# Performance work log

Measured on AMD Instinct MI355X. Metric: run time of the kernel, lower is better.

## Reference

```python
import jax, jax.numpy as jnp
import numpy as np

B, S, IN, D, H, L, DFF, C = 64, 256, 32, 512, 8, 2, 2048, 16
DH = D // H


def setup_inputs() -> dict:
    key = jax.random.key(0)
    ks = iter(jax.random.split(key, 40))
    r = lambda shp, s=0.02: (jax.random.normal(next(ks), shp, dtype=jnp.float32) * s)
    inp = {
        'x': jax.random.normal(next(ks), (B, S, IN), dtype=jnp.float32),
        'W_emb': r((IN, D)), 'b_emb': jnp.zeros((D,), jnp.float32),
        'Wq': r((L, D, D)), 'bq': jnp.zeros((L, D), jnp.float32),
        'Wk': r((L, D, D)), 'bk': jnp.zeros((L, D), jnp.float32),
        'Wv': r((L, D, D)), 'bv': jnp.zeros((L, D), jnp.float32),
        'Wo': r((L, D, D)), 'bo': jnp.zeros((L, D), jnp.float32),
        'ln1_s': jnp.ones((L, D), jnp.float32), 'ln1_b': jnp.zeros((L, D), jnp.float32),
        'W1': r((L, D, DFF)), 'b1': jnp.zeros((L, DFF), jnp.float32),
        'W2': r((L, DFF, D)), 'b2': jnp.zeros((L, D), jnp.float32),
        'ln2_s': jnp.ones((L, D), jnp.float32), 'ln2_b': jnp.zeros((L, D), jnp.float32),
        'e1_w': r((D, 128)), 'e1_b': jnp.zeros((128,), jnp.float32),
        'e2_w': r((128, D)), 'e2_b': jnp.zeros((D,), jnp.float32),
        'd1_w': r((D, 128)), 'd1_b': jnp.zeros((128,), jnp.float32),
        'd2_w': r((128, D)), 'd2_b': jnp.zeros((D,), jnp.float32),
        'y': jax.random.randint(next(ks), (B, S, 1), 0, C, dtype=jnp.int32),
    }
    return inp


def _ln(x, s, b):
    m = x.mean(-1, keepdims=True)
    v = ((x - m) ** 2).mean(-1, keepdims=True)
    return (x - m) / jnp.sqrt(v + 1e-5) * s + b


def _ari(a, t, n_cls):
    # adjusted rand index from contingency matrix (labels in [0, n_cls))
    idx = a * n_cls + t
    cm = jnp.zeros((n_cls * n_cls,), jnp.float32).at[idx].add(1.0).reshape(n_cls, n_cls)
    comb2 = lambda m: m * (m - 1.0) * 0.5
    sij = comb2(cm).sum()
    sa = comb2(cm.sum(1)).sum()
    sb = comb2(cm.sum(0)).sum()
    n = jnp.float32(a.shape[0])
    exp = sa * sb / (n * (n - 1.0) * 0.5)
    mx = 0.5 * (sa + sb)
    return (sij - exp) / (mx - exp)


def _net(x, W_emb, b_emb, Wq, bq, Wk, bk, Wv, bv, Wo, bo, ln1_s, ln1_b,
         W1, b1, W2, b2, ln2_s, ln2_b, e1_w, e1_b, e2_w, e2_b, d1_w, d1_b, d2_w, d2_b):
    h = x @ W_emb + b_emb  # [B,S,D]
    for l in range(L):
        q = (h @ Wq[l] + bq[l]).reshape(B, S, H, DH)
        k = (h @ Wk[l] + bk[l]).reshape(B, S, H, DH)
        v = (h @ Wv[l] + bv[l]).reshape(B, S, H, DH)
        scores = jnp.einsum('bqhd,bkhd->bhqk', q, k) / jnp.sqrt(jnp.float32(DH))
        attn = jax.nn.softmax(scores, axis=-1)
        o = jnp.einsum('bhqk,bkhd->bqhd', attn, v).reshape(B, S, D)
        h = _ln(h + o @ Wo[l] + bo[l], ln1_s[l], ln1_b[l])
        f = jax.nn.relu(h @ W1[l] + b1[l]) @ W2[l] + b2[l]
        h = _ln(h + f, ln2_s[l], ln2_b[l])
    enc = jax.nn.relu(h @ e1_w + e1_b) @ e2_w + e2_b
    z = jax.nn.relu(enc @ d1_w + d1_b) @ d2_w + d2_b  # input_to_cluster [B,S,D]
    return z


def reference(x, W_emb, b_emb, Wq, bq, Wk, bk, Wv, bv, Wo, bo, ln1_s, ln1_b,
              W1, b1, W2, b2, ln2_s, ln2_b, e1_w, e1_b, e2_w, e2_b,
              d1_w, d1_b, d2_w, d2_b, y):
    z = _net(x, W_emb, b_emb, Wq, bq, Wk, bk, Wv, bv, Wo, bo, ln1_s, ln1_b,
             W1, b1, W2, b2, ln2_s, ln2_b, e1_w, e1_b, e2_w, e2_b, d1_w, d1_b, d2_w, d2_b)
    # pairwise squared distances across batch per timestep: [S,B,B]
    sq = jnp.sum(z * z, -1)                       # [B,S]
    gram = jnp.einsum('bsd,csd->sbc', z, z)       # [S,B,B]
    dist = sq.T[:, :, None] + sq.T[:, None, :] - 2.0 * gram
    p = jax.nn.softmax(-dist, axis=-1)
    _, knn = jax.lax.top_k(p, C)                  # [S,B,C]
    # tot_sum: rows of dist selected once per i where knn[s,b,i]==i
    counts = jnp.sum(knn == jnp.arange(C)[None, None, :], axis=-1)  # [S,B]
    tot_sum = jnp.sum(dist.sum(-1) * counts.astype(dist.dtype))
    # gather neighbor labels and take mode (ties -> smallest value, like torch.mode)
    y2 = y[..., 0]                                 # [B,S]
    labels = y2[knn, jnp.arange(S)[:, None, None]] # [S,B,C]
    cnt = jnp.sum(labels[..., None] == jnp.arange(C), axis=-2)      # [S,B,C]
    assigned = jnp.argmax(cnt, axis=-1).astype(jnp.int32).reshape(-1)  # S*B (row-major, as torch)
    y_true = y.reshape(-1)                         # B*S (as torch: mismatched order is faithful)
    ari = _ari(assigned, y_true, C)
    return tot_sum, ari, assigned, z
```

## Files before the change

### kernel.cpp

```cpp
#include <hip/hip_runtime.h>
#include <cstdint>
#include <cmath>

#define B_ 64
#define S_ 256
#define IN_ 32
#define D_ 512
#define H_ 8
#define L_ 2
#define DFF_ 2048
#define C_ 16
#define DH_ 64
#define NTOK (B_*S_)
#define HALF_ 8192

typedef __attribute__((ext_vector_type(8))) short bf16x8;
typedef __attribute__((ext_vector_type(4))) float f32x4;
typedef __attribute__((ext_vector_type(8))) ushort ushortx8;

__device__ __forceinline__ ushort bf16_rn(float x) {
    union { float f; uint32_t u; } v; v.f = x;
    uint32_t r = v.u + 0x7fffu + ((v.u >> 16) & 1u);
    return (ushort)(r >> 16);
}
__device__ __forceinline__ float bf16_f32(ushort h) {
    union { uint32_t u; float f; } v; v.u = ((uint32_t)h) << 16;
    return v.f;
}

#define GLDS(gp, lp) __builtin_amdgcn_global_load_lds( \
    (const __attribute__((address_space(1))) void*)(gp), \
    (__attribute__((address_space(3))) void*)(lp), 16, 0, 0)

__device__ __forceinline__ int xcd_swz(int lid, int nwg) {
    return (lid & 7) * (nwg >> 3) + (lid >> 3);
}

template<int MODE>
__global__ __launch_bounds__(256)
void gemm3(const ushort* __restrict__ Ahi, const ushort* __restrict__ Alo,
           const ushort* __restrict__ Bhi, const ushort* __restrict__ Blo,
           const float* __restrict__ bias,
           float* __restrict__ Cf, ushort* __restrict__ Chi, ushort* __restrict__ Clo,
           int M, int N, int K)
{
    __shared__ __align__(16) ushort Als[2][2][128*32];
    __shared__ __align__(16) ushort Bls[2][2][128*32];
    const int tid  = threadIdx.x;
    const int wave = tid >> 6, lane = tid & 63;
    const int nwg = gridDim.x * gridDim.y;
    const int swz = xcd_swz(blockIdx.y * gridDim.x + blockIdx.x, nwg);
    const int m0 = (swz / gridDim.x) << 7, n0 = (swz % gridDim.x) << 7;
    const int wr = wave >> 1, wc = wave & 1;

    const ushort* Ah = Ahi + (size_t)m0 * K;
    const ushort* Al = Alo + (size_t)m0 * K;
    const ushort* Bh = Bhi + (size_t)n0 * K;
    const ushort* Bl = Blo + (size_t)n0 * K;

    const int KT = K >> 5;

    f32x4 acc[4][4];
    #pragma unroll
    for (int m = 0; m < 4; ++m)
        #pragma unroll
        for (int n = 0; n < 4; ++n)
            acc[m][n] = (f32x4){0.f, 0.f, 0.f, 0.f};

    auto stage = [&](int buf, int kk) {
        #pragma unroll
        for (int i = 0; i < 2; ++i) {
            const int rbase = wave * 32 + i * 16;
            const int row   = rbase + (lane >> 2);
            const int slot  = (lane & 3) ^ ((row >> 1) & 3);
            GLDS(Ah + (size_t)row * K + kk + slot * 8, &Als[buf][0][rbase * 32]);
            GLDS(Al + (size_t)row * K + kk + slot * 8, &Als[buf][1][rbase * 32]);
            GLDS(Bh + (size_t)row * K + kk + slot * 8, &Bls[buf][0][rbase * 32]);
            GLDS(Bl + (size_t)row * K + kk + slot * 8, &Bls[buf][1][rbase * 32]);
        }
    };

    stage(0, 0);
    for (int t = 0; t < KT; ++t) {
        const int buf = t & 1;
        if (t + 1 < KT) {
            stage(buf ^ 1, (t + 1) << 5);
            asm volatile("s_waitcnt vmcnt(8)" ::: "memory");
        } else {
            asm volatile("s_waitcnt vmcnt(0)" ::: "memory");
        }
        __builtin_amdgcn_sched_barrier(0);
        __builtin_amdgcn_s_barrier();

        const int chunk = lane >> 4;
        bf16x8 afh[4], afl[4], bfh[4], bfl[4];
        #pragma unroll
        for (int m = 0; m < 4; ++m) {
            const int row = wr * 64 + m * 16 + (lane & 15);
            const int sl  = chunk ^ ((row >> 1) & 3);
            afh[m] = *(const bf16x8*)(&Als[buf][0][row * 32 + sl * 8]);
            afl[m] = *(const bf16x8*)(&Als[buf][1][row * 32 + sl * 8]);
        }
        #pragma unroll
        for (int n = 0; n < 4; ++n) {
            const int row = wc * 64 + n * 16 + (lane & 15);
            const int sl  = chunk ^ ((row >> 1) & 3);
            bfh[n] = *(const bf16x8*)(&Bls[buf][0][row * 32 + sl * 8]);
            bfl[n] = *(const bf16x8*)(&Bls[buf][1][row * 32 + sl * 8]);
        }
        #pragma unroll
        for (int m = 0; m < 4; ++m)
            #pragma unroll
            for (int n = 0; n < 4; ++n) {
                acc[m][n] = __builtin_amdgcn_mfma_f32_16x16x32_bf16(afh[m], bfh[n], acc[m][n], 0, 0, 0);
                acc[m][n] = __builtin_amdgcn_mfma_f32_16x16x32_bf16(afh[m], bfl[n], acc[m][n], 0, 0, 0);
                acc[m][n] = __builtin_amdgcn_mfma_f32_16x16x32_bf16(afl[m], bfh[n], acc[m][n], 0, 0, 0);
            }
        __builtin_amdgcn_sched_barrier(0);
        __builtin_amdgcn_s_barrier();
    }

    const int col_l = lane & 15;
    float bv[4];
    #pragma unroll
    for (int n = 0; n < 4; ++n) bv[n] = bias[n0 + wc * 64 + n * 16 + col_l];
    #pragma unroll
    for (int m = 0; m < 4; ++m) {
        #pragma unroll
        for (int j = 0; j < 4; ++j) {
            const size_t grow = (size_t)(m0 + wr * 64 + m * 16 + (lane >> 4) * 4 + j);
            #pragma unroll
            for (int n = 0; n < 4; ++n) {
                float x = acc[m][n][j] + bv[n];
                if (MODE & 1) x = fmaxf(x, 0.f);
                const size_t gidx = grow * N + (n0 + wc * 64 + n * 16 + col_l);
                if (MODE < 2) {
                    Cf[gidx] = x;
                } else {
                    ushort hb = bf16_rn(x);
                    Chi[gidx] = hb;
                    Clo[gidx] = bf16_rn(x - bf16_f32(hb));
                }
            }
        }
    }
}

__global__ __launch_bounds__(256)
void qk_gemm(const ushort* __restrict__ qkvhi, const ushort* __restrict__ qkvlo,
             float* __restrict__ S)
{
    __shared__ __align__(16) ushort Als[2][2][128*32];
    __shared__ __align__(16) ushort Bls[2][2][128*32];
    const int tid = threadIdx.x, wave = tid >> 6, lane = tid & 63;
    const int swz = xcd_swz(blockIdx.y * 4 + blockIdx.x, 512);
    const int bh = swz >> 2;
    const int qt = (swz >> 1) & 1, kt = swz & 1;
    const int b = bh >> 3, h = bh & 7;
    const ushort* Ah = qkvhi + ((size_t)(b * 256 + qt * 128)) * 1536 + h * 64;
    const ushort* Al = qkvlo + ((size_t)(b * 256 + qt * 128)) * 1536 + h * 64;
    const ushort* Bh = qkvhi + ((size_t)(b * 256 + kt * 128)) * 1536 + 512 + h * 64;
    const ushort* Bl = qkvlo + ((size_t)(b * 256 + kt * 128)) * 1536 + 512 + h * 64;
    const int wr = wave >> 1, wc = wave & 1;

    f32x4 acc[4][4];
    #pragma unroll
    for (int m = 0; m < 4; ++m)
        #pragma unroll
        for (int n = 0; n < 4; ++n)
            acc[m][n] = (f32x4){0.f, 0.f, 0.f, 0.f};

    auto stage = [&](int buf, int kk) {
        #pragma unroll
        for (int i = 0; i < 2; ++i) {
            const int rbase = wave * 32 + i * 16;
            const int row   = rbase + (lane >> 2);
            const int slot  = (lane & 3) ^ ((row >> 1) & 3);
            GLDS(Ah + (size_t)row * 1536 + kk + slot * 8, &Als[buf][0][rbase * 32]);
            GLDS(Al + (size_t)row * 1536 + kk + slot * 8, &Als[buf][1][rbase * 32]);
            GLDS(Bh + (size_t)row * 1536 + kk + slot * 8, &Bls[buf][0][rbase * 32]);
            GLDS(Bl + (size_t)row * 1536 + kk + slot * 8, &Bls[buf][1][rbase * 32]);
        }
    };

    stage(0, 0);
    #pragma unroll
    for (int t = 0; t < 2; ++t) {
        __syncthreads();
        if (t == 0) stage(1, 32);
        const int chunk = lane >> 4;
        bf16x8 afh[4], afl[4], bfh[4], bfl[4];
        #pragma unroll
        for (int m = 0; m < 4; ++m) {
            const int row = wr * 64 + m * 16 + (lane & 15);
            const int sl  = chunk ^ ((row >> 1) & 3);
            afh[m] = *(const bf16x8*)(&Als[t][0][row * 32 + sl * 8]);
            afl[m] = *(const bf16x8*)(&Als[t][1][row * 32 + sl * 8]);
        }
        #pragma unroll
        for (int n = 0; n < 4; ++n) {
            const int row = wc * 64 + n * 16 + (lane & 15);
            const int sl  = chunk ^ ((row >> 1) & 3);
            bfh[n] = *(const bf16x8*)(&Bls[t][0][row * 32 + sl * 8]);
            bfl[n] = *(const bf16x8*)(&Bls[t][1][row * 32 + sl * 8]);
        }
        #pragma unroll
        for (int m = 0; m < 4; ++m)
            #pragma unroll
            for (int n = 0; n < 4; ++n) {
                acc[m][n] = __builtin_amdgcn_mfma_f32_16x16x32_bf16(afh[m], bfh[n], acc[m][n], 0, 0, 0);
                acc[m][n] = __builtin_amdgcn_mfma_f32_16x16x32_bf16(afh[m], bfl[n], acc[m][n], 0, 0, 0);
                acc[m][n] = __builtin_amdgcn_mfma_f32_16x16x32_bf16(afl[m], bfh[n], acc[m][n], 0, 0, 0);
            }
        __syncthreads();
    }

    const int col_l = lane & 15;
    #pragma unroll
    for (int m = 0; m < 4; ++m)
        #pragma unroll
        for (int j = 0; j < 4; ++j) {
            const int row = qt * 128 + wr * 64 + m * 16 + (lane >> 4) * 4 + j;
            #pragma unroll
            for (int n = 0; n < 4; ++n) {
                const int col = kt * 128 + wc * 64 + n * 16 + col_l;
                S[(size_t)bh * 65536 + (size_t)row * 256 + col] = acc[m][n][j] * 0.125f;
            }
        }
}

__global__ __launch_bounds__(256)
void softmax_p(const float* __restrict__ S, ushort* __restrict__ Phi,
               ushort* __restrict__ Plo)
{
    const int row = blockIdx.x * 4 + (threadIdx.x >> 6);
    const int lane = threadIdx.x & 63;
    float4 v = *(const float4*)(S + (size_t)row * 256 + lane * 4);
    float mx = fmaxf(fmaxf(v.x, v.y), fmaxf(v.z, v.w));
    #pragma unroll
    for (int d = 1; d < 64; d <<= 1) mx = fmaxf(mx, __shfl_xor(mx, d));
    float e0 = expf(v.x - mx), e1 = expf(v.y - mx);
    float e2 = expf(v.z - mx), e3 = expf(v.w - mx);
    float s = (e0 + e1) + (e2 + e3);
    #pragma unroll
    for (int d = 1; d < 64; d <<= 1) s += __shfl_xor(s, d);
    const float inv = 1.0f / s;
    float p0 = e0 * inv, p1 = e1 * inv, p2 = e2 * inv, p3 = e3 * inv;
    ushort4 hh, ll;
    hh.x = bf16_rn(p0); ll.x = bf16_rn(p0 - bf16_f32(hh.x));
    hh.y = bf16_rn(p1); ll.y = bf16_rn(p1 - bf16_f32(hh.y));
    hh.z = bf16_rn(p2); ll.z = bf16_rn(p2 - bf16_f32(hh.z));
    hh.w = bf16_rn(p3); ll.w = bf16_rn(p3 - bf16_f32(hh.w));
    *(ushort4*)(Phi + (size_t)row * 256 + lane * 4) = hh;
    *(ushort4*)(Plo + (size_t)row * 256 + lane * 4) = ll;
}

__global__ __launch_bounds__(256)
void vtrans(const ushort* __restrict__ qkvhi, const ushort* __restrict__ qkvlo,
            ushort* __restrict__ VThi, ushort* __restrict__ VTlo)
{
    __shared__ ushort T[64][272];
    const int bh = blockIdx.x;
    const int b = bh >> 3, h = bh & 7;
    const int tid = threadIdx.x;
    #pragma unroll
    for (int pass = 0; pass < 2; ++pass) {
        const ushort* src = pass ? qkvlo : qkvhi;
        ushort* dst = pass ? VTlo : VThi;
        const ushort* p = src + ((size_t)b * 256 + tid) * 1536 + 1024 + h * 64;
        #pragma unroll
        for (int i = 0; i < 8; ++i) {
            ushortx8 v = *(const ushortx8*)(p + i * 8);
            #pragma unroll
            for (int j = 0; j < 8; ++j) T[i * 8 + j][tid] = v[j];
        }
        __syncthreads();
        const int dh = tid >> 2, k0 = (tid & 3) * 64;
        ushort* op = dst + ((size_t)bh * 64 + dh) * 256 + k0;
        #pragma unroll
        for (int i = 0; i < 8; ++i)
            *(ushortx8*)(op + i * 8) = *(const ushortx8*)&T[dh][k0 + i * 8];
        __syncthreads();
    }
}

__global__ __launch_bounds__(256)
void pv_gemm(const ushort* __restrict__ Phi, const ushort* __restrict__ Plo,
             const ushort* __restrict__ VThi, const ushort* __restrict__ VTlo,
             ushort* __restrict__ obhi, ushort* __restrict__ oblo, int t0)
{
    __shared__ __align__(16) ushort Als[2][2][128*32];
    __shared__ __align__(16) ushort Bls[2][2][64*32];
    const int tid = threadIdx.x, wave = tid >> 6, lane = tid & 63;
    const int swz = xcd_swz(blockIdx.y * 2 + blockIdx.x, 256);
    const int bh = swz >> 1, qt = swz & 1;
    const ushort* Ah = Phi + ((size_t)bh * 256 + qt * 128) * 256;
    const ushort* Al = Plo + ((size_t)bh * 256 + qt * 128) * 256;
    const ushort* Bh = VThi + (size_t)bh * 64 * 256;
    const ushort* Bl = VTlo + (size_t)bh * 64 * 256;

    f32x4 acc[2][4];
    #pragma unroll
    for (int m = 0; m < 2; ++m)
        #pragma unroll
        for (int n = 0; n < 4; ++n)
            acc[m][n] = (f32x4){0.f, 0.f, 0.f, 0.f};

    auto stage = [&](int buf, int kk) {
        #pragma unroll
        for (int i = 0; i < 2; ++i) {
            const int rbase = wave * 32 + i * 16;
            const int row   = rbase + (lane >> 2);
            const int slot  = (lane & 3) ^ ((row >> 1) & 3);
            GLDS(Ah + (size_t)row * 256 + kk + slot * 8, &Als[buf][0][rbase * 32]);
            GLDS(Al + (size_t)row * 256 + kk + slot * 8, &Als[buf][1][rbase * 32]);
        }
        const int rbase2 = wave * 16;
        const int row2   = rbase2 + (lane >> 2);
        const int slot2  = (lane & 3) ^ ((row2 >> 1) & 3);
        GLDS(Bh + (size_t)row2 * 256 + kk + slot2 * 8, &Bls[buf][0][rbase2 * 32]);
        GLDS(Bl + (size_t)row2 * 256 + kk + slot2 * 8, &Bls[buf][1][rbase2 * 32]);
    };

    stage(0, 0);
    for (int t = 0; t < 8; ++t) {
        const int buf = t & 1;
        __syncthreads();
        if (t < 7) stage(buf ^ 1, (t + 1) << 5);
        const int chunk = lane >> 4;
        bf16x8 afh[2], afl[2], bfh[4], bfl[4];
        #pragma unroll
        for (int m = 0; m < 2; ++m) {
            const int row = wave * 32 + m * 16 + (lane & 15);
            const int sl  = chunk ^ ((row >> 1) & 3);
            afh[m] = *(const bf16x8*)(&Als[buf][0][row * 32 + sl * 8]);
            afl[m] = *(const bf16x8*)(&Als[buf][1][row * 32 + sl * 8]);
        }
        #pragma unroll
        for (int n = 0; n < 4; ++n) {
            const int row = n * 16 + (lane & 15);
            const int sl  = chunk ^ ((row >> 1) & 3);
            bfh[n] = *(const bf16x8*)(&Bls[buf][0][row * 32 + sl * 8]);
            bfl[n] = *(const bf16x8*)(&Bls[buf][1][row * 32 + sl * 8]);
        }
        #pragma unroll
        for (int m = 0; m < 2; ++m)
            #pragma unroll
            for (int n = 0; n < 4; ++n) {
                acc[m][n] = __builtin_amdgcn_mfma_f32_16x16x32_bf16(afh[m], bfh[n], acc[m][n], 0, 0, 0);
                acc[m][n] = __builtin_amdgcn_mfma_f32_16x16x32_bf16(afh[m], bfl[n], acc[m][n], 0, 0, 0);
                acc[m][n] = __builtin_amdgcn_mfma_f32_16x16x32_bf16(afl[m], bfh[n], acc[m][n], 0, 0, 0);
            }
        __syncthreads();
    }

    const int b = bh >> 3, h = bh & 7;
    const int col_l = lane & 15;
    #pragma unroll
    for (int m = 0; m < 2; ++m)
        #pragma unroll
        for (int j = 0; j < 4; ++j) {
            const int q = qt * 128 + wave * 32 + m * 16 + (lane >> 4) * 4 + j;
            const size_t token = (size_t)t0 + (size_t)b * 256 + q;
            #pragma unroll
            for (int n = 0; n < 4; ++n) {
                const int col = h * 64 + n * 16 + col_l;
                float x = acc[m][n][j];
                ushort hb = bf16_rn(x);
                obhi[token * 512 + col] = hb;
                oblo[token * 512 + col] = bf16_rn(x - bf16_f32(hb));
            }
        }
}

__global__ __launch_bounds__(256)
void gemm_f32(const float* __restrict__ A, const float* __restrict__ W,
              const float* __restrict__ bias, float* __restrict__ Cc,
              ushort* __restrict__ Chi, ushort* __restrict__ Clo,
              int M, int N, int K)
{
    __shared__ float As[16][68];
    __shared__ float Bs[16][64];
    const int tid = threadIdx.x;
    const int tx = tid & 15, ty = tid >> 4;
    const int m0 = blockIdx.y << 6, n0 = blockIdx.x << 6;
    const int arow = tid >> 2, ak4 = (tid & 3) << 2;
    const int brow = tid >> 4, bc4 = (tid & 15) << 2;
    float acc[4][4] = {};
    const float* aptr = A + (size_t)(m0 + arow) * K + ak4;
    const float* bptr = W + (size_t)brow * N + n0 + bc4;
    for (int k0 = 0; k0 < K; k0 += 16) {
        float4 av = *(const float4*)(aptr + k0);
        float4 bv = *(const float4*)(bptr + (size_t)k0 * N);
        __syncthreads();
        As[ak4+0][arow] = av.x; As[ak4+1][arow] = av.y;
        As[ak4+2][arow] = av.z; As[ak4+3][arow] = av.w;
        *(float4*)&Bs[brow][bc4] = bv;
        __syncthreads();
        #pragma unroll
        for (int kk = 0; kk < 16; ++kk) {
            float4 a = *(const float4*)&As[kk][ty << 2];
            float4 b = *(const float4*)&Bs[kk][tx << 2];
            float ar[4] = {a.x,a.y,a.z,a.w};
            float br[4] = {b.x,b.y,b.z,b.w};
            #pragma unroll
            for (int i = 0; i < 4; ++i)
                #pragma unroll
                for (int j = 0; j < 4; ++j)
                    acc[i][j] = fmaf(ar[i], br[j], acc[i][j]);
        }
    }
    float4 bb = *(const float4*)(bias + n0 + (tx << 2));
    #pragma unroll
    for (int i = 0; i < 4; ++i) {
        int m = m0 + (ty << 2) + i;
        float o[4];
        o[0] = acc[i][0] + bb.x; o[1] = acc[i][1] + bb.y;
        o[2] = acc[i][2] + bb.z; o[3] = acc[i][3] + bb.w;
        ushort4 hh, ll;
        hh.x = bf16_rn(o[0]); ll.x = bf16_rn(o[0] - bf16_f32(hh.x));
        hh.y = bf16_rn(o[1]); ll.y = bf16_rn(o[1] - bf16_f32(hh.y));
        hh.z = bf16_rn(o[2]); ll.z = bf16_rn(o[2] - bf16_f32(hh.z));
        hh.w = bf16_rn(o[3]); ll.w = bf16_rn(o[3] - bf16_f32(hh.w));
        const size_t base = (size_t)m * N + n0 + (tx << 2);
        *(float4*)(Cc + base) = (float4){o[0],o[1],o[2],o[3]};
        *(ushort4*)(Chi + base) = hh;
        *(ushort4*)(Clo + base) = ll;
    }
}

__global__ __launch_bounds__(256)
void transpose_split(const float* __restrict__ W, ushort* __restrict__ Thi,
                     ushort* __restrict__ Tlo, int K, int N)
{
    __shared__ float T[64][65];
    const int k0 = blockIdx.y << 6, n0 = blockIdx.x << 6;
    const int tid = threadIdx.x;
    #pragma unroll
    for (int i = 0; i < 16; ++i) {
        int idx = tid + i * 256;
        int kl = idx >> 6, nl = idx & 63;
        T[nl][kl] = W[(size_t)(k0 + kl) * N + n0 + nl];
    }
    __syncthreads();
    #pragma unroll
    for (int i = 0; i < 16; ++i) {
        int idx = tid + i * 256;
        int nl = idx >> 6, kl = idx & 63;
        float x = T[nl][kl];
        ushort hb = bf16_rn(x);
        size_t o = (size_t)(n0 + nl) * K + k0 + kl;
        Thi[o] = hb;
        Tlo[o] = bf16_rn(x - bf16_f32(hb));
    }
}

__global__ __launch_bounds__(256)
void concat3(const float* __restrict__ a, const float* __restrict__ b,
             const float* __restrict__ c, float* __restrict__ out)
{
    int i = blockIdx.x * 256 + threadIdx.x;
    out[i] = (i < 512) ? a[i] : (i < 1024 ? b[i - 512] : c[i - 1024]);
}

__global__ __launch_bounds__(64)
void ln_res(float* __restrict__ h, const float* __restrict__ t,
            const float* __restrict__ sc, const float* __restrict__ bi,
            ushort* __restrict__ hhi, ushort* __restrict__ hlo)
{
    const int row = blockIdx.x, lane = threadIdx.x;
    const size_t off = (size_t)row * D_ + (size_t)lane * 8;
    float x[8];
    float4 a0 = *(const float4*)(h + off),  a1 = *(const float4*)(h + off + 4);
    float4 b0 = *(const float4*)(t + off),  b1 = *(const float4*)(t + off + 4);
    x[0]=a0.x+b0.x; x[1]=a0.y+b0.y; x[2]=a0.z+b0.z; x[3]=a0.w+b0.w;
    x[4]=a1.x+b1.x; x[5]=a1.y+b1.y; x[6]=a1.z+b1.z; x[7]=a1.w+b1.w;

    float s = 0.f;
    #pragma unroll
    for (int i = 0; i < 8; ++i) s += x[i];
    #pragma unroll
    for (int d = 1; d < 64; d <<= 1) s += __shfl_xor(s, d);
    float mean = s * (1.0f / 512.0f);

    float vsum = 0.f;
    #pragma unroll
    for (int i = 0; i < 8; ++i) { float dx = x[i] - mean; vsum += dx * dx; }
    #pragma unroll
    for (int d = 1; d < 64; d <<= 1) vsum += __shfl_xor(vsum, d);
    float den = sqrtf(vsum * (1.0f / 512.0f) + 1e-5f);

    float4 s0 = *(const float4*)(sc + lane*8), s1 = *(const float4*)(sc + lane*8 + 4);
    float4 c0 = *(const float4*)(bi + lane*8), c1 = *(const float4*)(bi + lane*8 + 4);
    float scv[8] = {s0.x,s0.y,s0.z,s0.w,s1.x,s1.y,s1.z,s1.w};
    float biv[8] = {c0.x,c0.y,c0.z,c0.w,c1.x,c1.y,c1.z,c1.w};
    float out[8];
    ushort hh[8], ll[8];
    #pragma unroll
    for (int i = 0; i < 8; ++i) {
        out[i] = (x[i] - mean) / den * scv[i] + biv[i];
        hh[i] = bf16_rn(out[i]);
        ll[i] = bf16_rn(out[i] - bf16_f32(hh[i]));
    }
    *(float4*)(h + off)     = (float4){out[0],out[1],out[2],out[3]};
    *(float4*)(h + off + 4) = (float4){out[4],out[5],out[6],out[7]};
    *(ushort4*)(hhi + off)     = (ushort4){hh[0],hh[1],hh[2],hh[3]};
    *(ushort4*)(hhi + off + 4) = (ushort4){hh[4],hh[5],hh[6],hh[7]};
    *(ushort4*)(hlo + off)     = (ushort4){ll[0],ll[1],ll[2],ll[3]};
    *(ushort4*)(hlo + off + 4) = (ushort4){ll[4],ll[5],ll[6],ll[7]};
}

__global__ __launch_bounds__(64)
void sq_kernel(const float* __restrict__ z, float* __restrict__ sq)
{
#pragma clang fp contract(off)
    const int row = blockIdx.x, lane = threadIdx.x;
    const float* p = z + (size_t)row * D_ + (size_t)lane * 8;
    float4 a0 = *(const float4*)(p), a1 = *(const float4*)(p + 4);
    float s = 0.f;
    float vv[8] = {a0.x,a0.y,a0.z,a0.w,a1.x,a1.y,a1.z,a1.w};
    #pragma unroll
    for (int i = 0; i < 8; ++i) { float t = vv[i] * vv[i]; s = s + t; }
    #pragma unroll
    for (int d = 1; d < 64; d <<= 1) s += __shfl_xor(s, d);
    if (lane == 0) sq[row] = s;
}

__global__ __launch_bounds__(256)
void copy_z(const float* __restrict__ z, float* __restrict__ out)
{
    size_t i4 = (size_t)blockIdx.x * 256 + threadIdx.x;
    if (i4 < (size_t)NTOK * D_ / 4) {
        float4 t = ((const float4*)z)[i4];
        out[i4*4+0] = t.x; out[i4*4+1] = t.y;
        out[i4*4+2] = t.z; out[i4*4+3] = t.w;
    }
}

__global__ __launch_bounds__(256)
void gram_kernel(const float* __restrict__ z, float* __restrict__ gram)
{
    __shared__ float Ls[16][68];
    const int s = blockIdx.x;
    const int tid = threadIdx.x;
    const int tx = tid & 15, ty = tid >> 4;
    const int arow = tid >> 2, ak4 = (tid & 3) << 2;
    float acc[4][4] = {};
    const float* zp = z + ((size_t)arow * S_ + s) * D_ + ak4;
    for (int k0 = 0; k0 < D_; k0 += 16) {
        float4 av = *(const float4*)(zp + k0);
        __syncthreads();
        Ls[ak4+0][arow] = av.x; Ls[ak4+1][arow] = av.y;
        Ls[ak4+2][arow] = av.z; Ls[ak4+3][arow] = av.w;
        __syncthreads();
        #pragma unroll
        for (int kk = 0; kk < 16; ++kk) {
            float4 a = *(const float4*)&Ls[kk][ty << 2];
            float4 b = *(const float4*)&Ls[kk][tx << 2];
            float ar[4] = {a.x,a.y,a.z,a.w};
            float br[4] = {b.x,b.y,b.z,b.w};
            #pragma unroll
            for (int i = 0; i < 4; ++i)
                #pragma unroll
                for (int j = 0; j < 4; ++j)
                    acc[i][j] = fmaf(ar[i], br[j], acc[i][j]);
        }
    }
    #pragma unroll
    for (int i = 0; i < 4; ++i) {
        float4 o = {acc[i][0], acc[i][1], acc[i][2], acc[i][3]};
        *(float4*)(gram + ((size_t)s * 64 + (ty<<2) + i) * 64 + (tx<<2)) = o;
    }
}

__global__ __launch_bounds__(64)
void cluster_kernel(const float* __restrict__ gram, const float* __restrict__ sq,
                    const int* __restrict__ y, float* __restrict__ contrib,
                    int* __restrict__ assigned, float* __restrict__ out_assigned_f)
{
#pragma clang fp contract(off)
    __shared__ float G[64][65];
    __shared__ float sqs[64];
    const int s = blockIdx.x, b = threadIdx.x;
    for (int i = b; i < 4096; i += 64)
        G[i >> 6][i & 63] = gram[(size_t)s * 4096 + i];
    sqs[b] = sq[(size_t)b * S_ + s];
    __syncthreads();

    const float sqb = sqs[b];
    float dmin = INFINITY, dsum = 0.f;
    for (int c = 0; c < 64; ++c) {
        float d = sqb + sqs[c] - 2.0f * G[b][c];
        dmin = fminf(dmin, d);
        dsum = dsum + d;
    }
    float Z = 0.f;
    for (int c = 0; c < 64; ++c) {
        float d = sqb + sqs[c] - 2.0f * G[b][c];
        float e = expf(dmin - d);
        G[b][c] = e;
        Z = Z + e;
    }
    for (int c = 0; c < 64; ++c) G[b][c] = G[b][c] / Z;

    int knn[16];
    #pragma unroll
    for (int j = 0; j < 16; ++j) {
        float bp = -1.f; int bi2 = 0;
        for (int c = 0; c < 64; ++c) {
            float pv = G[b][c];
            if (pv > bp) { bp = pv; bi2 = c; }
        }
        knn[j] = bi2;
        G[b][bi2] = -1.f;
    }
    int cmatch = 0;
    #pragma unroll
    for (int j = 0; j < 16; ++j) cmatch += (knn[j] == j) ? 1 : 0;
    int lab[16];
    #pragma unroll
    for (int j = 0; j < 16; ++j) lab[j] = y[knn[j] * S_ + s];
    int bestc = -1, bestcls = 0;
    #pragma unroll
    for (int cls = 0; cls < 16; ++cls) {
        int cc = 0;
        #pragma unroll
        for (int j = 0; j < 16; ++j) cc += (lab[j] == cls) ? 1 : 0;
        if (cc > bestc) { bestc = cc; bestcls = cls; }
    }
    const int oi = s * 64 + b;
    contrib[oi] = dsum * (float)cmatch;
    assigned[oi] = bestcls;
    out_assigned_f[oi] = (float)bestcls;
}

__global__ __launch_bounds__(256)
void finalize_kernel(const float* __restrict__ contrib, const int* __restrict__ assigned,
                     const int* __restrict__ y, float* __restrict__ dout)
{
#pragma clang fp contract(off)
    __shared__ int cm[256];
    __shared__ float red[256];
    const int tid = threadIdx.x;
    cm[tid] = 0;
    float s = 0.f;
    for (int i = tid; i < NTOK; i += 256) s = s + contrib[i];
    red[tid] = s;
    __syncthreads();
    for (int i = tid; i < NTOK; i += 256)
        atomicAdd(&cm[assigned[i] * 16 + y[i]], 1);
    __syncthreads();
    for (int st = 128; st > 0; st >>= 1) {
        if (tid < st) red[tid] = red[tid] + red[tid + st];
        __syncthreads();
    }
    if (tid == 0) {
        dout[0] = red[0];
        float sij = 0.f, sa = 0.f, sb = 0.f;
        for (int i = 0; i < 256; ++i) {
            float mm = (float)cm[i];
            sij = sij + mm * (mm - 1.0f) * 0.5f;
        }
        for (int r = 0; r < 16; ++r) {
            int rs = 0;
            for (int c2 = 0; c2 < 16; ++c2) rs += cm[r * 16 + c2];
            float mm = (float)rs;
            sa = sa + mm * (mm - 1.0f) * 0.5f;
        }
        for (int c2 = 0; c2 < 16; ++c2) {
            int cs = 0;
            for (int r = 0; r < 16; ++r) cs += cm[r * 16 + c2];
            float mm = (float)cs;
            sb = sb + mm * (mm - 1.0f) * 0.5f;
        }
        float n = 16384.0f;
        float expv = sa * sb / (n * (n - 1.0f) * 0.5f);
        float mx = 0.5f * (sa + sb);
        dout[1] = (sij - expv) / (mx - expv);
    }
}

extern "C" void kernel_launch(void* const* d_in, const int* in_sizes, int n_in,
                              void* d_out, int out_size, void* d_ws, size_t ws_size,
                              hipStream_t stream)
{
    (void)in_sizes; (void)n_in; (void)out_size; (void)ws_size;
    const float* x     = (const float*)d_in[0];
    const float* W_emb = (const float*)d_in[1];
    const float* b_emb = (const float*)d_in[2];
    const float* Wq    = (const float*)d_in[3];
    const float* bq    = (const float*)d_in[4];
    const float* Wk    = (const float*)d_in[5];
    const float* bk    = (const float*)d_in[6];
    const float* Wv    = (const float*)d_in[7];
    const float* bv    = (const float*)d_in[8];
    const float* Wo    = (const float*)d_in[9];
    const float* bo    = (const float*)d_in[10];
    const float* ln1_s = (const float*)d_in[11];
    const float* ln1_b = (const float*)d_in[12];
    const float* W1    = (const float*)d_in[13];
    const float* b1    = (const float*)d_in[14];
    const float* W2    = (const float*)d_in[15];
    const float* b2    = (const float*)d_in[16];
    const float* ln2_s = (const float*)d_in[17];
    const float* ln2_b = (const float*)d_in[18];
    const float* e1_w  = (const float*)d_in[19];
    const float* e1_b  = (const float*)d_in[20];
    const float* e2_w  = (const float*)d_in[21];
    const float* e2_b  = (const float*)d_in[22];
    const float* d1_w  = (const float*)d_in[23];
    const float* d1_b  = (const float*)d_in[24];
    const float* d2_w  = (const float*)d_in[25];
    const float* d2_b  = (const float*)d_in[26];
    const int*   y     = (const int*)d_in[27];

    float* ws = (float*)d_ws;
    float*  h    = ws;
    ushort* hhi  = (ushort*)(ws + 8388608);
    ushort* hlo  = (ushort*)(ws + 12582912);
    float*  SCR  = ws + 16777216;
    ushort* obhi = (ushort*)(ws + 37748736);
    ushort* oblo = (ushort*)(ws + 41943040);
    float*  wt   = ws + 46137344;
    ushort* WTQKV_HI = (ushort*)wt;
    ushort* WTQKV_LO = WTQKV_HI + 786432;
    ushort* WTO_HI   = WTQKV_LO + 786432;
    ushort* WTO_LO   = WTO_HI + 262144;
    ushort* WT1_HI   = WTO_LO + 262144;
    ushort* WT1_LO   = WT1_HI + 1048576;
    ushort* WT2_HI   = WT1_LO + 1048576;
    ushort* WT2_LO   = WT2_HI + 1048576;
    ushort* WE1_HI   = WT2_LO + 1048576;
    ushort* WE1_LO   = WE1_HI + 65536;
    ushort* WE2_HI   = WE1_LO + 65536;
    ushort* WE2_LO   = WE2_HI + 65536;
    ushort* WD1_HI   = WE2_LO + 65536;
    ushort* WD1_LO   = WD1_HI + 65536;
    ushort* WD2_HI   = WD1_LO + 65536;
    ushort* WD2_LO   = WD2_HI + 65536;
    float*  biasqkv  = ws + 49545216;

    float*  Sb    = SCR;
    ushort* qkvhi = (ushort*)(SCR + 8388608);
    ushort* qkvlo = (ushort*)(SCR + 11534336);
    ushort* VThi  = (ushort*)(SCR + 14680064);
    ushort* VTlo  = (ushort*)(SCR + 15728640);
    ushort* Phi_  = (ushort*)(SCR + 8388608);
    ushort* Plo_  = (ushort*)(SCR + 16777216);
    float*  Of32  = SCR;
    ushort* f1hi  = (ushort*)SCR;
    ushort* f1lo  = (ushort*)(SCR + 8388608);
    float*  Xhalf = SCR + 16777216;
    ushort* enchi = (ushort*)SCR;
    ushort* enclo = (ushort*)(SCR + 4194304);
    float*  z     = SCR + 8388608;
    float*  gram  = SCR + 16777216;
    float*  sqb_  = SCR + 17825792;
    float*  contrib = SCR + 17842176;
    int*    assigned = (int*)(SCR + 17858560);
    ushort* t1hi = obhi;
    ushort* t1lo = oblo;
    ushort* t2hi = obhi + 2097152;
    ushort* t2lo = oblo + 2097152;
    float*  dout = (float*)d_out;

    dim3 blk(256);
    auto gg = [](int M, int N) { return dim3(N >> 7, M >> 7); };

    transpose_split<<<dim3(2, 8), blk, 0, stream>>>(e1_w, WE1_HI, WE1_LO, 512, 128);
    transpose_split<<<dim3(8, 2), blk, 0, stream>>>(e2_w, WE2_HI, WE2_LO, 128, 512);
    transpose_split<<<dim3(2, 8), blk, 0, stream>>>(d1_w, WD1_HI, WD1_LO, 512, 128);
    transpose_split<<<dim3(8, 2), blk, 0, stream>>>(d2_w, WD2_HI, WD2_LO, 128, 512);

    gemm_f32<<<dim3(8, 256), blk, 0, stream>>>(x, W_emb, b_emb, h, hhi, hlo, NTOK, D_, IN_);

    for (int l = 0; l < L_; ++l) {
        transpose_split<<<dim3(8, 8), blk, 0, stream>>>(Wq + (size_t)l*D_*D_, WTQKV_HI,            WTQKV_LO,            512, 512);
        transpose_split<<<dim3(8, 8), blk, 0, stream>>>(Wk + (size_t)l*D_*D_, WTQKV_HI + 512*512,  WTQKV_LO + 512*512,  512, 512);
        transpose_split<<<dim3(8, 8), blk, 0, stream>>>(Wv + (size_t)l*D_*D_, WTQKV_HI + 1024*512, WTQKV_LO + 1024*512, 512, 512);
        transpose_split<<<dim3(8, 8), blk, 0, stream>>>(Wo + (size_t)l*D_*D_, WTO_HI, WTO_LO, 512, 512);
        transpose_split<<<dim3(32, 8), blk, 0, stream>>>(W1 + (size_t)l*D_*DFF_, WT1_HI, WT1_LO, 512, 2048);
        transpose_split<<<dim3(8, 32), blk, 0, stream>>>(W2 + (size_t)l*DFF_*D_, WT2_HI, WT2_LO, 2048, 512);
        concat3<<<dim3(6), blk, 0, stream>>>(bq + l*D_, bk + l*D_, bv + l*D_, biasqkv);

        for (int qtr = 0; qtr < 4; ++qtr) {
            const size_t hoff = (size_t)qtr * 4096 * 512;
            gemm3<2><<<gg(4096, 1536), blk, 0, stream>>>(
                hhi + hoff, hlo + hoff, WTQKV_HI, WTQKV_LO, biasqkv,
                nullptr, qkvhi, qkvlo, 4096, 1536, 512);
            vtrans<<<dim3(128), blk, 0, stream>>>(qkvhi, qkvlo, VThi, VTlo);
            qk_gemm<<<dim3(4, 128), blk, 0, stream>>>(qkvhi, qkvlo, Sb);
            softmax_p<<<dim3(8192), blk, 0, stream>>>(Sb, Phi_, Plo_);
            pv_gemm<<<dim3(2, 128), blk, 0, stream>>>(Phi_, Plo_, VThi, VTlo,
                                                      obhi, oblo, qtr * 4096);
        }
        gemm3<0><<<gg(NTOK, 512), blk, 0, stream>>>(
            obhi, oblo, WTO_HI, WTO_LO, bo + l*D_,
            Of32, nullptr, nullptr, NTOK, 512, 512);
        ln_res<<<dim3(NTOK), dim3(64), 0, stream>>>(h, Of32, ln1_s + l*D_, ln1_b + l*D_, hhi, hlo);

        for (int half = 0; half < 2; ++half) {
            const size_t ro = (size_t)half * HALF_ * D_;
            gemm3<3><<<gg(HALF_, DFF_), blk, 0, stream>>>(
                hhi + ro, hlo + ro, WT1_HI, WT1_LO, b1 + l*DFF_,
                nullptr, f1hi, f1lo, HALF_, 2048, 512);
            gemm3<0><<<gg(HALF_, 512), blk, 0, stream>>>(
                f1hi, f1lo, WT2_HI, WT2_LO, b2 + l*D_,
                Xhalf, nullptr, nullptr, HALF_, 512, 2048);
            ln_res<<<dim3(HALF_), dim3(64), 0, stream>>>(
                h + ro, Xhalf, ln2_s + l*D_, ln2_b + l*D_, hhi + ro, hlo + ro);
        }
    }

    gemm3<3><<<gg(NTOK, 128), blk, 0, stream>>>(
        hhi, hlo, WE1_HI, WE1_LO, e1_b, nullptr, t1hi, t1lo, NTOK, 128, 512);
    gemm3<2><<<gg(NTOK, 512), blk, 0, stream>>>(
        t1hi, t1lo, WE2_HI, WE2_LO, e2_b, nullptr, enchi, enclo, NTOK, 512, 128);
    gemm3<3><<<gg(NTOK, 128), blk, 0, stream>>>(
        enchi, enclo, WD1_HI, WD1_LO, d1_b, nullptr, t2hi, t2lo, NTOK, 128, 512);
    gemm3<0><<<gg(NTOK, 512), blk, 0, stream>>>(
        t2hi, t2lo, WD2_HI, WD2_LO, d2_b, z, nullptr, nullptr, NTOK, 512, 128);

    copy_z<<<dim3(NTOK * D_ / 4 / 256), blk, 0, stream>>>(z, dout + 16386);
    sq_kernel<<<dim3(NTOK), dim3(64), 0, stream>>>(z, sqb_);
    gram_kernel<<<dim3(S_), blk, 0, stream>>>(z, gram);
    cluster_kernel<<<dim3(S_), dim3(64), 0, stream>>>(gram, sqb_, y, contrib, assigned, dout + 2);
    finalize_kernel<<<dim3(1), blk, 0, stream>>>(contrib, assigned, y, dout);
}
```

Before: 1.570 ms.

## Add 256x256-tile 512-thread split-bf16 GEMM with phased pipeline for FFN1

```diff
diff --git a/kernel.cpp b/kernel.cpp
--- a/kernel.cpp
+++ b/kernel.cpp
@@ -34,6 +34,141 @@
 
 __device__ __forceinline__ int xcd_swz(int lid, int nwg) {
     return (lid & 7) * (nwg >> 3) + (lid >> 3);
+}
+
+template<int MODE>
+__global__ __launch_bounds__(512)
+void gemm3_8p(const ushort* __restrict__ Ahi, const ushort* __restrict__ Alo,
+              const ushort* __restrict__ Bhi, const ushort* __restrict__ Blo,
+              const float* __restrict__ bias,
+              float* __restrict__ Cf, ushort* __restrict__ Chi, ushort* __restrict__ Clo,
+              int M, int N, int K)
+{
+    __shared__ __align__(16) ushort Als[2][2][128*64];
+    __shared__ __align__(16) ushort Bls[2][2][128*64];
+    const int tid = threadIdx.x, wave = tid >> 6, lane = tid & 63;
+    const int nwg = gridDim.x * gridDim.y;
+    const int swz = xcd_swz(blockIdx.y * gridDim.x + blockIdx.x, nwg);
+    const int m0 = (swz / gridDim.x) << 8, n0 = (swz % gridDim.x) << 8;
+    const int wr = wave >> 2, wc = wave & 3;
+
+    const ushort* Ahp = Ahi + (size_t)m0 * K;
+    const ushort* Alp = Alo + (size_t)m0 * K;
+    const ushort* Bhp = Bhi + (size_t)n0 * K;
+    const ushort* Blp = Blo + (size_t)n0 * K;
+
+    const int KT = K >> 6;
+    const int NT = 3 * KT;
+
+    f32x4 acc[8][4];
+    #pragma unroll
+    for (int m = 0; m < 8; ++m)
+        #pragma unroll
+        for (int n = 0; n < 4; ++n)
+            acc[m][n] = (f32x4){0.f, 0.f, 0.f, 0.f};
+
+    auto stage_part = [&](int buf, const ushort* Asrc, const ushort* Bsrc,
+                          int kk, int part) {
+        const int hf = part & 1;
+        const ushort* src = (part < 2) ? Asrc : Bsrc;
+        ushort* dstbase = (part < 2) ? &Als[buf][hf][0] : &Bls[buf][hf][0];
+        #pragma unroll
+        for (int j = 0; j < 2; ++j) {
+            const int rl   = wave * 16 + j * 8 + (lane >> 3);
+            const int slot = (lane & 7) ^ (rl & 7);
+            GLDS(src + (size_t)(hf * 128 + rl) * K + kk + slot * 8,
+                 dstbase + (wave * 16 + j * 8) * 64);
+        }
+    };
+
+    #pragma unroll
+    for (int part = 0; part < 4; ++part)
+        stage_part(0, Ahp, Bhp, 0, part);
+
+    int seg = 0, kt = 0;
+    for (int g = 0; g < NT; ++g) {
+        const int buf = g & 1;
+        int nseg = seg, nkt = kt + 1;
+        if (nkt == KT) { nkt = 0; nseg = seg + 1; }
+        const ushort* An = (nseg == 2) ? Alp : Ahp;
+        const ushort* Bn = (nseg == 1) ? Blp : Bhp;
+        const bool more = (g + 1 < NT);
+
+        bf16x8 bfr[4][2];
+        #pragma unroll
+        for (int p = 0; p < 4; ++p) {
+            if (more) stage_part(buf ^ 1, An, Bn, nkt << 6, p);
+            if (p == 0) {
+                if (more) asm volatile("s_waitcnt vmcnt(2)" ::: "memory");
+                else      asm volatile("s_waitcnt vmcnt(0)" ::: "memory");
+                __builtin_amdgcn_sched_barrier(0);
+                __builtin_amdgcn_s_barrier();
+                #pragma unroll
+                for (int nj = 0; nj < 4; ++nj) {
+                    const int gr = wc * 64 + nj * 16;
+                    const int hb2 = gr >> 7;
+                    const int rl = (gr & 127) + (lane & 15);
+                    #pragma unroll
+                    for (int ks = 0; ks < 2; ++ks) {
+                        const int es = (ks * 4 + (lane >> 4)) ^ (lane & 7);
+                        bfr[nj][ks] = *(const bf16x8*)&Bls[buf][hb2][rl * 64 + es * 8];
+                    }
+                }
+            }
+            bf16x8 a0[2], a1[2];
+            {
+                const int r0 = (2 * p) * 16 + (lane & 15);
+                const int r1 = (2 * p + 1) * 16 + (lane & 15);
+                #pragma unroll
+                for (int ks = 0; ks < 2; ++ks) {
+                    const int es = (ks * 4 + (lane >> 4)) ^ (lane & 7);
+                    a0[ks] = *(const bf16x8*)&Als[buf][wr][r0 * 64 + es * 8];
+                    a1[ks] = *(const bf16x8*)&Als[buf][wr][r1 * 64 + es * 8];
+                }
+            }
+            __builtin_amdgcn_sched_barrier(0);
+            __builtin_amdgcn_s_barrier();
+            asm volatile("s_waitcnt lgkmcnt(0)" ::: "memory");
+            __builtin_amdgcn_sched_barrier(0);
+            __builtin_amdgcn_s_setprio(1);
+            #pragma unroll
+            for (int ks = 0; ks < 2; ++ks)
+                #pragma unroll
+                for (int nj = 0; nj < 4; ++nj) {
+                    acc[2*p][nj]   = __builtin_amdgcn_mfma_f32_16x16x32_bf16(a0[ks], bfr[nj][ks], acc[2*p][nj],   0, 0, 0);
+                    acc[2*p+1][nj] = __builtin_amdgcn_mfma_f32_16x16x32_bf16(a1[ks], bfr[nj][ks], acc[2*p+1][nj], 0, 0, 0);
+                }
+            __builtin_amdgcn_s_setprio(0);
+            __builtin_amdgcn_sched_barrier(0);
+            __builtin_amdgcn_s_barrier();
+        }
+        seg = nseg; kt = nkt;
+    }
+
+    const int col_l = lane & 15;
+    float bv[4];
+    #pragma unroll
+    for (int nj = 0; nj < 4; ++nj) bv[nj] = bias[n0 + wc * 64 + nj * 16 + col_l];
+    #pragma unroll
+    for (int mi = 0; mi < 8; ++mi) {
+        #pragma unroll
+        for (int jj = 0; jj < 4; ++jj) {
+            const size_t grow = (size_t)(m0 + wr * 128 + mi * 16 + (lane >> 4) * 4 + jj);
+            #pragma unroll
+            for (int nj = 0; nj < 4; ++nj) {
+                float x = acc[mi][nj][jj] + bv[nj];
+                if (MODE & 1) x = fmaxf(x, 0.f);
+                const size_t gidx = grow * N + (n0 + wc * 64 + nj * 16 + col_l);
+                if (MODE < 2) {
+                    Cf[gidx] = x;
+                } else {
+                    ushort hb = bf16_rn(x);
+                    Chi[gidx] = hb;
+                    Clo[gidx] = bf16_rn(x - bf16_f32(hb));
+                }
+            }
+        }
+    }
 }
 
 template<int MODE>
@@ -801,7 +936,7 @@
 
         for (int half = 0; half < 2; ++half) {
             const size_t ro = (size_t)half * HALF_ * D_;
-            gemm3<3><<<gg(HALF_, DFF_), blk, 0, stream>>>(
+            gemm3_8p<3><<<dim3(DFF_ >> 8, HALF_ >> 8), dim3(512), 0, stream>>>(
                 hhi + ro, hlo + ro, WT1_HI, WT1_LO, b1 + l*DFF_,
                 nullptr, f1hi, f1lo, HALF_, 2048, 512);
             gemm3<0><<<gg(HALF_, 512), blk, 0, stream>>>(
```

After: 1.676 ms. +6.8%, slower.

## Fuse QK^T score GEMM with softmax and pack four LayerNorm rows per block

Applied to the files above, without the earlier changes.

```diff
diff --git a/kernel.cpp b/kernel.cpp
--- a/kernel.cpp
+++ b/kernel.cpp
@@ -147,112 +147,127 @@
 }
 
 __global__ __launch_bounds__(256)
-void qk_gemm(const ushort* __restrict__ qkvhi, const ushort* __restrict__ qkvlo,
-             float* __restrict__ S)
-{
-    __shared__ __align__(16) ushort Als[2][2][128*32];
-    __shared__ __align__(16) ushort Bls[2][2][128*32];
+void qks_gemm(const ushort* __restrict__ qkvhi, const ushort* __restrict__ qkvlo,
+              ushort* __restrict__ Phi, ushort* __restrict__ Plo)
+{
+    __shared__ __align__(16) ushort Qls[2][128*64];
+    __shared__ __align__(16) ushort Kls[2][128*64];
     const int tid = threadIdx.x, wave = tid >> 6, lane = tid & 63;
-    const int swz = xcd_swz(blockIdx.y * 4 + blockIdx.x, 512);
-    const int bh = swz >> 2;
-    const int qt = (swz >> 1) & 1, kt = swz & 1;
+    const int swz = xcd_swz(blockIdx.y * 2 + blockIdx.x, 256);
+    const int bh = swz >> 1, qt = swz & 1;
     const int b = bh >> 3, h = bh & 7;
-    const ushort* Ah = qkvhi + ((size_t)(b * 256 + qt * 128)) * 1536 + h * 64;
-    const ushort* Al = qkvlo + ((size_t)(b * 256 + qt * 128)) * 1536 + h * 64;
-    const ushort* Bh = qkvhi + ((size_t)(b * 256 + kt * 128)) * 1536 + 512 + h * 64;
-    const ushort* Bl = qkvlo + ((size_t)(b * 256 + kt * 128)) * 1536 + 512 + h * 64;
-    const int wr = wave >> 1, wc = wave & 1;
-
-    f32x4 acc[4][4];
-    #pragma unroll
-    for (int m = 0; m < 4; ++m)
-        #pragma unroll
-        for (int n = 0; n < 4; ++n)
-            acc[m][n] = (f32x4){0.f, 0.f, 0.f, 0.f};
-
-    auto stage = [&](int buf, int kk) {
-        #pragma unroll
-        for (int i = 0; i < 2; ++i) {
-            const int rbase = wave * 32 + i * 16;
-            const int row   = rbase + (lane >> 2);
-            const int slot  = (lane & 3) ^ ((row >> 1) & 3);
-            GLDS(Ah + (size_t)row * 1536 + kk + slot * 8, &Als[buf][0][rbase * 32]);
-            GLDS(Al + (size_t)row * 1536 + kk + slot * 8, &Als[buf][1][rbase * 32]);
-            GLDS(Bh + (size_t)row * 1536 + kk + slot * 8, &Bls[buf][0][rbase * 32]);
-            GLDS(Bl + (size_t)row * 1536 + kk + slot * 8, &Bls[buf][1][rbase * 32]);
+
+    const ushort* Qh = qkvhi + ((size_t)(b * 256 + qt * 128)) * 1536 + h * 64;
+    const ushort* Ql = qkvlo + ((size_t)(b * 256 + qt * 128)) * 1536 + h * 64;
+    const ushort* Kh = qkvhi + ((size_t)(b * 256)) * 1536 + 512 + h * 64;
+    const ushort* Kl = qkvlo + ((size_t)(b * 256)) * 1536 + 512 + h * 64;
+
+    auto stage128 = [&](const ushort* src, ushort* dst) {
+        #pragma unroll
+        for (int j = 0; j < 4; ++j) {
+            const int rl   = j * 32 + wave * 8 + (lane >> 3);
+            const int slot = (lane & 7) ^ (rl & 7);
+            GLDS(src + (size_t)rl * 1536 + slot * 8, dst + (j * 32 + wave * 8) * 64);
         }
     };
 
-    stage(0, 0);
-    #pragma unroll
-    for (int t = 0; t < 2; ++t) {
-        __syncthreads();
-        if (t == 0) stage(1, 32);
-        const int chunk = lane >> 4;
-        bf16x8 afh[4], afl[4], bfh[4], bfl[4];
-        #pragma unroll
-        for (int m = 0; m < 4; ++m) {
-            const int row = wr * 64 + m * 16 + (lane & 15);
-            const int sl  = chunk ^ ((row >> 1) & 3);
-            afh[m] = *(const bf16x8*)(&Als[t][0][row * 32 + sl * 8]);
-            afl[m] = *(const bf16x8*)(&Als[t][1][row * 32 + sl * 8]);
-        }
-        #pragma unroll
-        for (int n = 0; n < 4; ++n) {
-            const int row = wc * 64 + n * 16 + (lane & 15);
-            const int sl  = chunk ^ ((row >> 1) & 3);
-            bfh[n] = *(const bf16x8*)(&Bls[t][0][row * 32 + sl * 8]);
-            bfl[n] = *(const bf16x8*)(&Bls[t][1][row * 32 + sl * 8]);
-        }
-        #pragma unroll
-        for (int m = 0; m < 4; ++m)
-            #pragma unroll
-            for (int n = 0; n < 4; ++n) {
-                acc[m][n] = __builtin_amdgcn_mfma_f32_16x16x32_bf16(afh[m], bfh[n], acc[m][n], 0, 0, 0);
-                acc[m][n] = __builtin_amdgcn_mfma_f32_16x16x32_bf16(afh[m], bfl[n], acc[m][n], 0, 0, 0);
-                acc[m][n] = __builtin_amdgcn_mfma_f32_16x16x32_bf16(afl[m], bfh[n], acc[m][n], 0, 0, 0);
+    f32x4 acc[2][16];
+    #pragma unroll
+    for (int mi = 0; mi < 2; ++mi)
+        #pragma unroll
+        for (int nj = 0; nj < 16; ++nj)
+            acc[mi][nj] = (f32x4){0.f, 0.f, 0.f, 0.f};
+
+    stage128(Qh, &Qls[0][0]);
+    stage128(Ql, &Qls[1][0]);
+    stage128(Kh, &Kls[0][0]);
+    stage128(Kl, &Kls[1][0]);
+    asm volatile("s_waitcnt vmcnt(0)" ::: "memory");
+    __builtin_amdgcn_sched_barrier(0);
+    __builtin_amdgcn_s_barrier();
+
+    bf16x8 qh[2][2], ql[2][2];
+    #pragma unroll
+    for (int mi = 0; mi < 2; ++mi)
+        #pragma unroll
+        for (int ks = 0; ks < 2; ++ks) {
+            const int row = wave * 32 + mi * 16 + (lane & 15);
+            const int es  = (ks * 4 + (lane >> 4)) ^ (lane & 7);
+            qh[mi][ks] = *(const bf16x8*)&Qls[0][row * 64 + es * 8];
+            ql[mi][ks] = *(const bf16x8*)&Qls[1][row * 64 + es * 8];
+        }
+
+    #pragma unroll
+    for (int hk = 0; hk < 2; ++hk) {
+        if (hk == 1) {
+            __syncthreads();
+            stage128(Kh + (size_t)128 * 1536, &Kls[0][0]);
+            stage128(Kl + (size_t)128 * 1536, &Kls[1][0]);
+            asm volatile("s_waitcnt vmcnt(0)" ::: "memory");
+            __builtin_amdgcn_sched_barrier(0);
+            __builtin_amdgcn_s_barrier();
+        }
+        #pragma unroll
+        for (int ng = 0; ng < 2; ++ng) {
+            bf16x8 kh[4][2], kl[4][2];
+            #pragma unroll
+            for (int nj = 0; nj < 4; ++nj)
+                #pragma unroll
+                for (int ks = 0; ks < 2; ++ks) {
+                    const int row = (ng * 4 + nj) * 16 + (lane & 15);
+                    const int es  = (ks * 4 + (lane >> 4)) ^ (lane & 7);
+                    kh[nj][ks] = *(const bf16x8*)&Kls[0][row * 64 + es * 8];
+                    kl[nj][ks] = *(const bf16x8*)&Kls[1][row * 64 + es * 8];
+                }
+            #pragma unroll
+            for (int mi = 0; mi < 2; ++mi)
+                #pragma unroll
+                for (int nj = 0; nj < 4; ++nj) {
+                    const int an = hk * 8 + ng * 4 + nj;
+                    #pragma unroll
+                    for (int ks = 0; ks < 2; ++ks) {
+                        acc[mi][an] = __builtin_amdgcn_mfma_f32_16x16x32_bf16(qh[mi][ks], kh[nj][ks], acc[mi][an], 0, 0, 0);
+                        acc[mi][an] = __builtin_amdgcn_mfma_f32_16x16x32_bf16(qh[mi][ks], kl[nj][ks], acc[mi][an], 0, 0, 0);
+                        acc[mi][an] = __builtin_amdgcn_mfma_f32_16x16x32_bf16(ql[mi][ks], kh[nj][ks], acc[mi][an], 0, 0, 0);
+                    }
+                }
+        }
+    }
+
+    const int colb = lane & 15;
+    #pragma unroll
+    for (int mi = 0; mi < 2; ++mi) {
+        #pragma unroll
+        for (int j = 0; j < 4; ++j) {
+            float v[16];
+            float mx = -INFINITY;
+            #pragma unroll
+            for (int nj = 0; nj < 16; ++nj) {
+                v[nj] = acc[mi][nj][j] * 0.125f;
+                mx = fmaxf(mx, v[nj]);
             }
-        __syncthreads();
-    }
-
-    const int col_l = lane & 15;
-    #pragma unroll
-    for (int m = 0; m < 4; ++m)
-        #pragma unroll
-        for (int j = 0; j < 4; ++j) {
-            const int row = qt * 128 + wr * 64 + m * 16 + (lane >> 4) * 4 + j;
-            #pragma unroll
-            for (int n = 0; n < 4; ++n) {
-                const int col = kt * 128 + wc * 64 + n * 16 + col_l;
-                S[(size_t)bh * 65536 + (size_t)row * 256 + col] = acc[m][n][j] * 0.125f;
+            #pragma unroll
+            for (int d = 1; d < 16; d <<= 1) mx = fmaxf(mx, __shfl_xor(mx, d));
+            float sum = 0.f;
+            #pragma unroll
+            for (int nj = 0; nj < 16; ++nj) {
+                v[nj] = expf(v[nj] - mx);
+                sum += v[nj];
             }
-        }
-}
-
-__global__ __launch_bounds__(256)
-void softmax_p(const float* __restrict__ S, ushort* __restrict__ Phi,
-               ushort* __restrict__ Plo)
-{
-    const int row = blockIdx.x * 4 + (threadIdx.x >> 6);
-    const int lane = threadIdx.x & 63;
-    float4 v = *(const float4*)(S + (size_t)row * 256 + lane * 4);
-    float mx = fmaxf(fmaxf(v.x, v.y), fmaxf(v.z, v.w));
-    #pragma unroll
-    for (int d = 1; d < 64; d <<= 1) mx = fmaxf(mx, __shfl_xor(mx, d));
-    float e0 = expf(v.x - mx), e1 = expf(v.y - mx);
-    float e2 = expf(v.z - mx), e3 = expf(v.w - mx);
-    float s = (e0 + e1) + (e2 + e3);
-    #pragma unroll
-    for (int d = 1; d < 64; d <<= 1) s += __shfl_xor(s, d);
-    const float inv = 1.0f / s;
-    float p0 = e0 * inv, p1 = e1 * inv, p2 = e2 * inv, p3 = e3 * inv;
-    ushort4 hh, ll;
-    hh.x = bf16_rn(p0); ll.x = bf16_rn(p0 - bf16_f32(hh.x));
-    hh.y = bf16_rn(p1); ll.y = bf16_rn(p1 - bf16_f32(hh.y));
-    hh.z = bf16_rn(p2); ll.z = bf16_rn(p2 - bf16_f32(hh.z));
-    hh.w = bf16_rn(p3); ll.w = bf16_rn(p3 - bf16_f32(hh.w));
-    *(ushort4*)(Phi + (size_t)row * 256 + lane * 4) = hh;
-    *(ushort4*)(Plo + (size_t)row * 256 + lane * 4) = ll;
+            #pragma unroll
+            for (int d = 1; d < 16; d <<= 1) sum += __shfl_xor(sum, d);
+            const float inv = 1.0f / sum;
+            const int qrow = qt * 128 + wave * 32 + mi * 16 + (lane >> 4) * 4 + j;
+            const size_t base = ((size_t)bh * 256 + qrow) * 256;
+            #pragma unroll
+            for (int nj = 0; nj < 16; ++nj) {
+                float p = v[nj] * inv;
+                ushort hb = bf16_rn(p);
+                Phi[base + nj * 16 + colb] = hb;
+                Plo[base + nj * 16 + colb] = bf16_rn(p - bf16_f32(hb));
+            }
+        }
+    }
 }
 
 __global__ __launch_bounds__(256)
@@ -463,12 +478,13 @@
     out[i] = (i < 512) ? a[i] : (i < 1024 ? b[i - 512] : c[i - 1024]);
 }
 
-__global__ __launch_bounds__(64)
+__global__ __launch_bounds__(256)
 void ln_res(float* __restrict__ h, const float* __restrict__ t,
             const float* __restrict__ sc, const float* __restrict__ bi,
             ushort* __restrict__ hhi, ushort* __restrict__ hlo)
 {
-    const int row = blockIdx.x, lane = threadIdx.x;
+    const int row = blockIdx.x * 4 + (threadIdx.x >> 6);
+    const int lane = threadIdx.x & 63;
     const size_t off = (size_t)row * D_ + (size_t)lane * 8;
     float x[8];
     float4 a0 = *(const float4*)(h + off),  a1 = *(const float4*)(h + off + 4);
@@ -740,13 +756,12 @@
     ushort* WD2_LO   = WD2_HI + 65536;
     float*  biasqkv  = ws + 49545216;
 
-    float*  Sb    = SCR;
+    ushort* Phi_  = (ushort*)SCR;
+    ushort* Plo_  = (ushort*)(SCR + 4194304);
     ushort* qkvhi = (ushort*)(SCR + 8388608);
     ushort* qkvlo = (ushort*)(SCR + 11534336);
     ushort* VThi  = (ushort*)(SCR + 14680064);
     ushort* VTlo  = (ushort*)(SCR + 15728640);
-    ushort* Phi_  = (ushort*)(SCR + 8388608);
-    ushort* Plo_  = (ushort*)(SCR + 16777216);
     float*  Of32  = SCR;
     ushort* f1hi  = (ushort*)SCR;
     ushort* f1lo  = (ushort*)(SCR + 8388608);
@@ -789,15 +804,14 @@
                 hhi + hoff, hlo + hoff, WTQKV_HI, WTQKV_LO, biasqkv,
                 nullptr, qkvhi, qkvlo, 4096, 1536, 512);
             vtrans<<<dim3(128), blk, 0, stream>>>(qkvhi, qkvlo, VThi, VTlo);
-            qk_gemm<<<dim3(4, 128), blk, 0, stream>>>(qkvhi, qkvlo, Sb);
-            softmax_p<<<dim3(8192), blk, 0, stream>>>(Sb, Phi_, Plo_);
+            qks_gemm<<<dim3(2, 128), blk, 0, stream>>>(qkvhi, qkvlo, Phi_, Plo_);
             pv_gemm<<<dim3(2, 128), blk, 0, stream>>>(Phi_, Plo_, VThi, VTlo,
                                                       obhi, oblo, qtr * 4096);
         }
         gemm3<0><<<gg(NTOK, 512), blk, 0, stream>>>(
             obhi, oblo, WTO_HI, WTO_LO, bo + l*D_,
             Of32, nullptr, nullptr, NTOK, 512, 512);
-        ln_res<<<dim3(NTOK), dim3(64), 0, stream>>>(h, Of32, ln1_s + l*D_, ln1_b + l*D_, hhi, hlo);
+        ln_res<<<dim3(NTOK / 4), blk, 0, stream>>>(h, Of32, ln1_s + l*D_, ln1_b + l*D_, hhi, hlo);
 
         for (int half = 0; half < 2; ++half) {
             const size_t ro = (size_t)half * HALF_ * D_;
@@ -807,7 +821,7 @@
             gemm3<0><<<gg(HALF_, 512), blk, 0, stream>>>(
                 f1hi, f1lo, WT2_HI, WT2_LO, b2 + l*D_,
                 Xhalf, nullptr, nullptr, HALF_, 512, 2048);
-            ln_res<<<dim3(HALF_), dim3(64), 0, stream>>>(
+            ln_res<<<dim3(HALF_ / 4), blk, 0, stream>>>(
                 h + ro, Xhalf, ln2_s + l*D_, ln2_b + l*D_, hhi + ro, hlo + ro);
         }
     }
```

New measurement: 1.500 ms. 4.5% less time.
